# Optimization experiments

Measured on AMD Instinct MI355X. Metric: run time of the kernel, lower is better.

The kernel has to match this reference:

```python
import jax, jax.numpy as jnp
import numpy as np

N = 10000          # nodes
E = 200000         # edges (avg degree 20)
LAT = 128          # latent dim
NEXP = 8           # experts
NTYPE = 95         # atom types (hard-coded 95x0e in module)
M0, M1, M2 = 128, 64, 32          # node/out irreps muls for l=0,1,2 (dim 480)
E0, E1, E2 = 64, 32, 16           # edge irreps muls (dim 240)
C0, C1, C2 = M0 + E0, M1 + E1, M2 + E2   # concat channels per l
T0 = M0 + M1 + M2                 # gate-input scalars: 128 scalars + 96 gates
AVG_NEIGH = 20.0


def setup_inputs() -> dict:
    key = jax.random.key(0)
    ks = jax.random.split(key, 32)
    r = lambda i, sh: jax.random.normal(ks[i], sh, dtype=jnp.float32)
    return {
        "latents": r(0, (E, LAT)),
        "node_features": r(1, (N, M0 + 3 * M1 + 5 * M2)),
        "edge_features": r(2, (E, E0 + 3 * E1 + 5 * E2)),
        "edge_vector": r(3, (E, 3)),
        "mole_globals": r(4, (LAT,)),
        "wigner_D1": r(5, (E, 3, 3)),
        "wigner_D2": r(6, (E, 5, 5)),
        "node_onehot": jax.nn.one_hot(jax.random.randint(ks[7], (N,), 0, NTYPE), NTYPE, dtype=jnp.float32),
        "Wg": r(8, (LAT, NEXP)),
        "Wm": r(9, (LAT, NEXP)),
        "W0_e": r(10, (NEXP, C0, T0)), "W0_s": r(11, (C0, T0)),
        "W1_e": r(12, (NEXP, C1, M1)), "W1_s": r(13, (C1, M1)),
        "W2_e": r(14, (NEXP, C2, M2)), "W2_s": r(15, (C2, M2)),
        "Wp0": r(16, (M0, M0)), "bp0": jnp.zeros((M0,), jnp.float32),
        "Wp1": r(17, (M1, M1)), "Wp2": r(18, (M2, M2)),
        "Wenv": r(19, (LAT, M0 + M1 + M2)),
        "Woh0": r(20, (M0, NTYPE)), "Woh1": r(21, (M1, NTYPE)), "Woh2": r(22, (M2, NTYPE)),
        "atom_type": jax.random.randint(ks[23], (N,), 0, NTYPE),
        "edge_index": jax.random.randint(ks[24], (2, E), 0, N),
        "active_edges": jnp.arange(E),
    }


def _mix(x, We, Ws, g):
    """Latent(expert)-conditioned per-l channel mixing: y = x @ (sum_e g_e W_e + W_shared).
    Loops over the small fixed expert count; never materializes per-edge weight matrices."""
    xm = x if x.ndim == 3 else x[:, :, None]           # [a, c, m]
    y = jnp.einsum('acm,co->aom', xm, Ws)
    for e in range(NEXP):
        y = y + g[:, e, None, None] * jnp.einsum('acm,co->aom', xm, We[e])
    y = y * float(1.0 / np.sqrt(xm.shape[1]))
    return y[:, :, 0] if x.ndim == 2 else y


def reference(latents, node_features, edge_features, edge_vector, mole_globals,
              wigner_D1, wigner_D2, node_onehot, Wg, Wm,
              W0_e, W0_s, W1_e, W1_s, W2_e, W2_s,
              Wp0, bp0, Wp1, Wp2, Wenv, Woh0, Woh1, Woh2,
              atom_type, edge_index, active_edges):
    edge_center = edge_index[0][active_edges]
    lat = latents[active_edges]
    # gather node features along edges, split irreps blocks
    xn = node_features[edge_center]                         # [Ea, 480]
    n0 = xn[:, :M0]
    n1 = xn[:, M0:M0 + 3 * M1].reshape(-1, M1, 3)
    n2 = xn[:, M0 + 3 * M1:].reshape(-1, M2, 5)
    e0 = edge_features[:, :E0]
    e1 = edge_features[:, E0:E0 + 3 * E1].reshape(-1, E1, 3)
    e2 = edge_features[:, E0 + 3 * E1:].reshape(-1, E2, 5)
    x0 = jnp.concatenate([n0, e0], axis=1)                  # [Ea, C0]
    x1 = jnp.concatenate([n1, e1], axis=1)                  # [Ea, C1, 3]
    x2 = jnp.concatenate([n2, e2], axis=1)                  # [Ea, C2, 5]
    # latent + molecular-global conditioned expert gates
    gates = jax.nn.softmax(lat @ Wg + mole_globals @ Wm, axis=-1)   # [Ea, NEXP]
    # SO(2)-style TP: rotate l>0 blocks into edge frame (Wigner-D), mix channels, rotate back
    x1r = jnp.einsum('amn,acn->acm', wigner_D1, x1)
    x2r = jnp.einsum('amn,acn->acm', wigner_D2, x2)
    t0 = _mix(x0, W0_e, W0_s, gates)                        # [Ea, T0]
    t1 = jnp.einsum('anm,aom->aon', wigner_D1, _mix(x1r, W1_e, W1_s, gates))
    t2 = jnp.einsum('anm,aom->aon', wigner_D2, _mix(x2r, W2_e, W2_s, gates))
    # Gate nonlinearity: silu scalars, sigmoid gates scale l>0 channels
    s = jax.nn.silu(t0[:, :M0])
    v1 = t1 * jax.nn.sigmoid(t0[:, M0:M0 + M1])[:, :, None]
    v2 = t2 * jax.nn.sigmoid(t0[:, M0 + M1:])[:, :, None]
    # lin_post: per-l equivariant linear (bias only on scalars), fan-in normalized
    s = s @ Wp0 * float(1.0 / np.sqrt(M0)) + bp0
    v1 = jnp.einsum('acm,co->aom', v1, Wp1) * float(1.0 / np.sqrt(M1))
    v2 = jnp.einsum('acm,co->aom', v2, Wp2) * float(1.0 / np.sqrt(M2))
    # E3ElementLinear: per-channel weights generated from latents
    w = lat @ Wenv * float(1.0 / np.sqrt(LAT))              # [Ea, M0+M1+M2]
    s = s * w[:, :M0]
    v1 = v1 * w[:, M0:M0 + M1, None]
    v2 = v2 * w[:, M0 + M1:, None]
    # scatter-reduce messages to nodes, normalize by rsqrt(avg_num_neighbors)
    norm = float(1.0 / np.sqrt(AVG_NEIGH))
    o0 = jax.ops.segment_sum(s, edge_center, num_segments=N) * norm
    o1 = jax.ops.segment_sum(v1, edge_center, num_segments=N) * norm
    o2 = jax.ops.segment_sum(v2, edge_center, num_segments=N) * norm
    # residual blend (res_update_params=0 -> u=sigmoid(0)=0.5), identity residual
    u = 0.5
    c_old = float(1.0 / np.sqrt(u * u + 1.0))
    c_new = u * c_old
    h0 = c_old * node_features[:, :M0] + c_new * o0
    h1 = c_old * node_features[:, M0:M0 + 3 * M1].reshape(N, M1, 3) + c_new * o1
    h2 = c_old * node_features[:, M0 + 3 * M1:].reshape(N, M2, 5) + c_new * o2
    # layer-onehot 'uvu' weighted TP with 95x0e, fan-in normalized, added residually
    invs = float(1.0 / np.sqrt(NTYPE))
    h0 = h0 + h0 * (node_onehot @ Woh0.T) * invs
    h1 = h1 + h1 * (node_onehot @ Woh1.T)[:, :, None] * invs
    h2 = h2 + h2 * (node_onehot @ Woh2.T)[:, :, None] * invs
    return jnp.concatenate([h0, h1.reshape(N, 3 * M1), h2.reshape(N, 5 * M2)], axis=1)
```

## Files before the change

kernel.cpp:

```cpp
#include <hip/hip_runtime.h>
#include <math.h>

namespace {

typedef __attribute__((ext_vector_type(8))) short short8;
typedef __attribute__((ext_vector_type(4))) float f32x4;

constexpr int kN   = 10000;
constexpr int kE   = 200000;
constexpr int kNT  = 95;
constexpr int kNFD = 480;

__device__ __forceinline__ ushort bf(float f) {
  union { float f; uint u; } c; c.f = f;
  uint r = c.u + 0x7FFF + ((c.u >> 16) & 1);
  return (ushort)(r >> 16);
}
__device__ __forceinline__ float fb(ushort u) {
  union { uint u; float f; } c; c.u = ((uint)u) << 16;
  return c.f;
}
__device__ __forceinline__ uint pk2(float a, float b) {
  return (uint)bf(a) | ((uint)bf(b) << 16);
}

__device__ __forceinline__ void packone(int u, const float* We, const float* Ws,
                                        int expStride, int Kreal, int N, int NT,
                                        int NKp, ushort* d) {
  int i = u & 7;
  int lane = (u >> 3) & 63;
  int rest = u >> 9;
  int kc = rest % NKp; rest /= NKp;
  int nt = rest % NT;
  int e  = rest / NT;
  int k = kc*32 + (lane >> 4)*8 + i;
  int n = nt*16 + (lane & 15);
  float v = 0.f;
  if (k < Kreal) {
    const float* s = (Ws != nullptr && e == 8) ? Ws : (We + (size_t)e*expStride);
    v = s[(size_t)k*N + n];
  }
  d[u] = bf(v);
}

constexpr int PK0   = 0;
constexpr int PK1   = 387072;
constexpr int PK2   = 442368;
constexpr int PKENV = 460800;
constexpr int PKP0  = 489472;
constexpr int PKP1  = 505856;
constexpr int PKP2  = 509952;
constexpr int PKTOT = 510976;

__global__ __launch_bounds__(256)
void pack_k(const float* __restrict__ W0e, const float* __restrict__ W0s,
            const float* __restrict__ W1e, const float* __restrict__ W1s,
            const float* __restrict__ W2e, const float* __restrict__ W2s,
            const float* __restrict__ Wenv, const float* __restrict__ Wp0,
            const float* __restrict__ Wp1, const float* __restrict__ Wp2,
            ushort* __restrict__ dst) {
  int gid = blockIdx.x*256 + threadIdx.x;
  if (gid >= PKTOT) return;
  if (gid < PK1)        packone(gid - PK0,   W0e, W0s, 192*224, 192, 224, 14, 6, dst + PK0);
  else if (gid < PK2)   packone(gid - PK1,   W1e, W1s, 96*64,    96,  64,  4, 3, dst + PK1);
  else if (gid < PKENV) packone(gid - PK2,   W2e, W2s, 48*32,    48,  32,  2, 2, dst + PK2);
  else if (gid < PKP0)  packone(gid - PKENV, Wenv, nullptr, 0,  128, 224, 14, 4, dst + PKENV);
  else if (gid < PKP1)  packone(gid - PKP0,  Wp0, nullptr, 0,   128, 128,  8, 4, dst + PKP0);
  else if (gid < PKP2)  packone(gid - PKP1,  Wp1, nullptr, 0,    64,  64,  4, 2, dst + PKP1);
  else                  packone(gid - PKP2,  Wp2, nullptr, 0,    32,  32,  2, 1, dst + PKP2);
}

__global__ __launch_bounds__(64)
void mgl_k(const float* __restrict__ mgv, const float* __restrict__ Wm,
           float* __restrict__ mgl) {
  int x = threadIdx.x;
  if (x < 8) {
    float s = 0.f;
    for (int l = 0; l < 128; ++l) s += mgv[l]*Wm[l*8 + x];
    mgl[x] = s;
  }
}

__global__ __launch_bounds__(256)
void hist_k(const int* __restrict__ eidx, const int* __restrict__ act,
            int* __restrict__ counts) {
  int e = blockIdx.x*256 + threadIdx.x;
  if (e < kE) atomicAdd(&counts[eidx[act[e]]], 1);
}

__global__ __launch_bounds__(256)
void scan_k(const int* __restrict__ counts, int* __restrict__ rowptr,
            int* __restrict__ cursor) {
  __shared__ int part[256];
  const int t = threadIdx.x;
  const int start = t*40;
  int local = 0;
  for (int i = 0; i < 40; ++i) {
    int idx = start + i;
    if (idx < kN) local += counts[idx];
  }
  part[t] = local;
  __syncthreads();
  for (int ofs = 1; ofs < 256; ofs <<= 1) {
    int v = (t >= ofs) ? part[t - ofs] : 0;
    __syncthreads();
    part[t] += v;
    __syncthreads();
  }
  int run = part[t] - local;
  for (int i = 0; i < 40; ++i) {
    int idx = start + i;
    if (idx < kN) {
      rowptr[idx] = run;
      cursor[idx] = run;
      run += counts[idx];
    }
  }
  if (t == 255) rowptr[kN] = run;
}

__global__ __launch_bounds__(256)
void scatter_k(const int* __restrict__ eidx, const int* __restrict__ act,
               int* __restrict__ cursor, int* __restrict__ elist) {
  int e = blockIdx.x*256 + threadIdx.x;
  if (e < kE) {
    int n = eidx[act[e]];
    int pos = atomicAdd(&cursor[n], 1);
    elist[pos] = e;
  }
}

__global__ __launch_bounds__(256)
void prep_k(const float* __restrict__ latents, const float* __restrict__ nodef,
            const float* __restrict__ edgef, const float* __restrict__ mgl,
            const float* __restrict__ D1, const float* __restrict__ D2,
            const float* __restrict__ Wg,
            const int* __restrict__ eidx, const int* __restrict__ act,
            float* __restrict__ coefg,
            ushort* __restrict__ x0, ushort* __restrict__ x1r,
            ushort* __restrict__ x2r) {
  __shared__ int aidl[32], cenl[32];
  const int tid = threadIdx.x;
  const int base = blockIdx.x*32;

  if (tid < 32) {
    int a = act[base + tid];
    aidl[tid] = a;
    cenl[tid] = eidx[a];
  }
  __syncthreads();

  {
    int e = tid >> 3, x = tid & 7;
    const float* lat = latents + (size_t)aidl[e]*128;
    float s = mgl[x];
    for (int l = 0; l < 128; ++l) s += lat[l]*Wg[l*8 + x];
    float mx = s;
    mx = fmaxf(mx, __shfl_xor(mx, 1));
    mx = fmaxf(mx, __shfl_xor(mx, 2));
    mx = fmaxf(mx, __shfl_xor(mx, 4));
    float ex = __expf(s - mx);
    float sm = ex;
    sm += __shfl_xor(sm, 1);
    sm += __shfl_xor(sm, 2);
    sm += __shfl_xor(sm, 4);
    size_t a = base + e;
    coefg[a*9 + x] = ex/sm;
    if (x == 0) coefg[a*9 + 8] = 1.f;
  }

  for (int u = tid; u < 32*24; u += 256) {
    int e = u/24, g = u - e*24;
    int c0 = g*8;
    size_t a = base + e;
    const float* s = (g < 16) ? (nodef + (size_t)cenl[e]*kNFD + c0)
                              : (edgef + a*240 + (c0 - 128));
    float4 f0 = *(const float4*)s;
    float4 f1 = *(const float4*)(s + 4);
    uint4 o;
    o.x = pk2(f0.x, f0.y); o.y = pk2(f0.z, f0.w);
    o.z = pk2(f1.x, f1.y); o.w = pk2(f1.z, f1.w);
    *(uint4*)(x0 + a*192 + c0) = o;
  }

  for (int u = tid; u < 32*36; u += 256) {
    int e = u/36, r = u - e*36;
    int mm = r/12, g = r - mm*12;
    int c0 = g*8;
    size_t a = base + e;
    const float* dd = D1 + a*9 + mm*3;
    const float* s = (g < 8) ? (nodef + (size_t)cenl[e]*kNFD + 128 + c0*3)
                             : (edgef + a*240 + 64 + (c0 - 64)*3);
    float ld[24];
    #pragma unroll
    for (int q = 0; q < 6; ++q)
      *(float4*)(ld + q*4) = *(const float4*)(s + q*4);
    float d0 = dd[0], d1 = dd[1], d2 = dd[2];
    float ov[8];
    #pragma unroll
    for (int j = 0; j < 8; ++j)
      ov[j] = d0*ld[3*j] + d1*ld[3*j + 1] + d2*ld[3*j + 2];
    uint4 o;
    o.x = pk2(ov[0], ov[1]); o.y = pk2(ov[2], ov[3]);
    o.z = pk2(ov[4], ov[5]); o.w = pk2(ov[6], ov[7]);
    *(uint4*)(x1r + (a*3 + mm)*96 + c0) = o;
  }

  for (int u = tid; u < 32*40; u += 256) {
    int e = u/40, r = u - e*40;
    int mm = r >> 3, g = r & 7;
    int c0 = g*8;
    size_t a = base + e;
    uint4 o = {0u,0u,0u,0u};
    if (g < 6) {
      const float* dd = D2 + a*25 + mm*5;
      const float* s = (g < 4) ? (nodef + (size_t)cenl[e]*kNFD + 320 + c0*5)
                               : (edgef + a*240 + 160 + (c0 - 32)*5);
      float ld[40];
      #pragma unroll
      for (int q = 0; q < 10; ++q)
        *(float4*)(ld + q*4) = *(const float4*)(s + q*4);
      float d0 = dd[0], d1 = dd[1], d2 = dd[2], d3 = dd[3], d4 = dd[4];
      float ov[8];
      #pragma unroll
      for (int j = 0; j < 8; ++j)
        ov[j] = d0*ld[5*j] + d1*ld[5*j+1] + d2*ld[5*j+2] + d3*ld[5*j+3] + d4*ld[5*j+4];
      o.x = pk2(ov[0], ov[1]); o.y = pk2(ov[2], ov[3]);
      o.z = pk2(ov[4], ov[5]); o.w = pk2(ov[6], ov[7]);
    }
    *(uint4*)(x2r + (a*5 + mm)*64 + c0) = o;
  }
}

constexpr int gemm_smbytes(int K1, int NK, int N, int NEXP) {
  int LDA = K1 + 8;
  int NT = N/16;
  int a = 128*LDA*2;
  int b = NT*NK*1024;
  int u = a > b ? a : b;
  return u + (NEXP > 1 ? 128*NEXP*4 : 0);
}

template<int DIV, int K1, int NK, int N, int NEXP, int EPI, bool AF32>
__global__ __launch_bounds__(512)
void gemm_k(const ushort* __restrict__ A, const float* __restrict__ Af,
            const int* __restrict__ ridx, int strideA,
            const ushort* __restrict__ Bpk, const float* __restrict__ coefg,
            int rowsReal, float norm,
            ushort* __restrict__ outbf, const float* __restrict__ bias,
            const ushort* __restrict__ wenvbf, int WCOL) {
  constexpr int NT  = N/16;
  constexpr int CTW = NT/2;
  constexpr int LDA = K1 + 8;
  constexpr int ABYTES = 128*LDA*2;
  constexpr int BBYTES = NT*NK*1024;
  constexpr int UNI = (ABYTES > BBYTES) ? ABYTES : BBYTES;

  extern __shared__ char smraw[];
  ushort* Asm = (ushort*)smraw;
  float* coefsm = (float*)(smraw + UNI);

  const int tid = threadIdx.x;
  const int row0 = blockIdx.x*128;

  constexpr int C8 = K1/8;
  for (int u = tid; u < 128*C8; u += 512) {
    int r = u / C8, c8 = u - r*C8;
    int gr = row0 + r;
    uint4 v = {0u,0u,0u,0u};
    if (gr < rowsReal) {
      if constexpr (AF32) {
        const float* s = Af + (size_t)(ridx ? ridx[gr] : gr)*strideA + c8*8;
        float4 f0 = *(const float4*)s;
        float4 f1 = *(const float4*)(s + 4);
        v.x = pk2(f0.x, f0.y); v.y = pk2(f0.z, f0.w);
        v.z = pk2(f1.x, f1.y); v.w = pk2(f1.z, f1.w);
      } else {
        v = *(const uint4*)(A + (size_t)gr*strideA + c8*8);
      }
    }
    *(uint4*)(&Asm[r*LDA + c8*8]) = v;
  }
  if constexpr (NEXP > 1) {
    for (int u = tid; u < 128*NEXP; u += 512) {
      int r = u / NEXP, e = u - r*NEXP;
      int a = (row0 + r)/DIV;
      coefsm[r*NEXP + e] = coefg[(size_t)a*NEXP + e];
    }
  }
  __syncthreads();

  const int lane = tid & 63, wid = tid >> 6;
  const int cg = wid & 1, rg = wid >> 1;
  const int rbase = rg*32;
  const int lrow = lane & 15, lkb = lane >> 4;

  short8 af[2][NK];
  #pragma unroll
  for (int rt = 0; rt < 2; ++rt)
    #pragma unroll
    for (int kc = 0; kc < NK; ++kc)
      af[rt][kc] = *(const short8*)(&Asm[(rbase + rt*16 + lrow)*LDA + kc*32 + lkb*8]);

  f32x4 acc[2][CTW];
  #pragma unroll
  for (int rt = 0; rt < 2; ++rt)
    #pragma unroll
    for (int ct = 0; ct < CTW; ++ct)
      acc[rt][ct] = f32x4{0.f,0.f,0.f,0.f};

  __syncthreads();

  union BU { uint4 u; short8 s; };
  uint4* Bsm4 = (uint4*)smraw;
  const uint4* Bg4 = (const uint4*)Bpk;

  for (int e = 0; e < NEXP; ++e) {
    for (int u = tid; u < NT*NK*64; u += 512)
      Bsm4[u] = Bg4[(size_t)e*(NT*NK*64) + u];
    __syncthreads();

    if constexpr (NEXP > 1) {
      float cf[2][4];
      #pragma unroll
      for (int rt = 0; rt < 2; ++rt)
        #pragma unroll
        for (int q = 0; q < 4; ++q)
          cf[rt][q] = coefsm[(rbase + rt*16 + lkb*4 + q)*NEXP + e];
      #pragma unroll
      for (int ct = 0; ct < CTW; ++ct) {
        int nt = cg*CTW + ct;
        f32x4 z[2];
        z[0] = f32x4{0.f,0.f,0.f,0.f};
        z[1] = f32x4{0.f,0.f,0.f,0.f};
        #pragma unroll
        for (int kc = 0; kc < NK; ++kc) {
          BU b; b.u = Bsm4[(nt*NK + kc)*64 + lane];
          z[0] = __builtin_amdgcn_mfma_f32_16x16x32_bf16(af[0][kc], b.s, z[0], 0, 0, 0);
          z[1] = __builtin_amdgcn_mfma_f32_16x16x32_bf16(af[1][kc], b.s, z[1], 0, 0, 0);
        }
        #pragma unroll
        for (int q = 0; q < 4; ++q) {
          acc[0][ct][q] += cf[0][q]*z[0][q];
          acc[1][ct][q] += cf[1][q]*z[1][q];
        }
      }
    } else {
      #pragma unroll
      for (int ct = 0; ct < CTW; ++ct) {
        int nt = cg*CTW + ct;
        #pragma unroll
        for (int kc = 0; kc < NK; ++kc) {
          BU b; b.u = Bsm4[(nt*NK + kc)*64 + lane];
          acc[0][ct] = __builtin_amdgcn_mfma_f32_16x16x32_bf16(af[0][kc], b.s, acc[0][ct], 0, 0, 0);
          acc[1][ct] = __builtin_amdgcn_mfma_f32_16x16x32_bf16(af[1][kc], b.s, acc[1][ct], 0, 0, 0);
        }
      }
    }
    __syncthreads();
  }

  #pragma unroll
  for (int rt = 0; rt < 2; ++rt) {
    #pragma unroll
    for (int ct = 0; ct < CTW; ++ct) {
      #pragma unroll
      for (int q = 0; q < 4; ++q) {
        int gr = row0 + rbase + rt*16 + lkb*4 + q;
        if (gr >= rowsReal) continue;
        int o = (cg*CTW + ct)*16 + lrow;
        float val = acc[rt][ct][q]*norm;
        if constexpr (EPI == 0) {
          outbf[(size_t)gr*N + o] = bf(val);
        } else if constexpr (EPI == 1) {
          float av = (o < 128) ? (val/(1.f + __expf(-val)))
                               : (1.f/(1.f + __expf(-val)));
          outbf[(size_t)gr*N + o] = bf(av);
        } else {
          int a = gr/DIV;
          if (bias != nullptr) val += bias[o];
          float w = fb(wenvbf[(size_t)a*224 + WCOL + o]);
          val *= w*0.22360679774997896f;
          outbf[(size_t)gr*N + o] = bf(val);
        }
      }
    }
  }
}

__global__ __launch_bounds__(256)
void mid_k(const ushort* __restrict__ y1, const ushort* __restrict__ y2,
           const ushort* __restrict__ t0act, const float* __restrict__ D1,
           const float* __restrict__ D2, ushort* __restrict__ v1,
           ushort* __restrict__ v2) {
  const int base = blockIdx.x*64;
  const int tid = threadIdx.x;

  for (int u = tid; u < 64*24; u += 256) {
    int e = u/24, r = u - e*24;
    int n = r >> 3, g = r & 7;
    int c0 = g*8;
    size_t a = base + e;
    const float* dd = D1 + a*9 + n*3;
    float d0 = dd[0], d1 = dd[1], d2 = dd[2];
    short8 m0 = *(const short8*)(y1 + ((size_t)a*3 + 0)*64 + c0);
    short8 m1 = *(const short8*)(y1 + ((size_t)a*3 + 1)*64 + c0);
    short8 m2 = *(const short8*)(y1 + ((size_t)a*3 + 2)*64 + c0);
    short8 gt = *(const short8*)(t0act + a*224 + 128 + c0);
    float ov[8];
    #pragma unroll
    for (int j = 0; j < 8; ++j) {
      float s = d0*fb((ushort)m0[j]) + d1*fb((ushort)m1[j]) + d2*fb((ushort)m2[j]);
      ov[j] = s*fb((ushort)gt[j]);
    }
    uint4 o;
    o.x = pk2(ov[0], ov[1]); o.y = pk2(ov[2], ov[3]);
    o.z = pk2(ov[4], ov[5]); o.w = pk2(ov[6], ov[7]);
    *(uint4*)(v1 + ((size_t)a*3 + n)*64 + c0) = o;
  }

  for (int u = tid; u < 64*20; u += 256) {
    int e = u/20, r = u - e*20;
    int n = r >> 2, g = r & 3;
    int c0 = g*8;
    size_t a = base + e;
    const float* dd = D2 + a*25 + n*5;
    short8 m0 = *(const short8*)(y2 + ((size_t)a*5 + 0)*32 + c0);
    short8 m1 = *(const short8*)(y2 + ((size_t)a*5 + 1)*32 + c0);
    short8 m2 = *(const short8*)(y2 + ((size_t)a*5 + 2)*32 + c0);
    short8 m3 = *(const short8*)(y2 + ((size_t)a*5 + 3)*32 + c0);
    short8 m4 = *(const short8*)(y2 + ((size_t)a*5 + 4)*32 + c0);
    short8 gt = *(const short8*)(t0act + a*224 + 192 + c0);
    float ov[8];
    #pragma unroll
    for (int j = 0; j < 8; ++j) {
      float s = dd[0]*fb((ushort)m0[j]) + dd[1]*fb((ushort)m1[j])
              + dd[2]*fb((ushort)m2[j]) + dd[3]*fb((ushort)m3[j])
              + dd[4]*fb((ushort)m4[j]);
      ov[j] = s*fb((ushort)gt[j]);
    }
    uint4 o;
    o.x = pk2(ov[0], ov[1]); o.y = pk2(ov[2], ov[3]);
    o.z = pk2(ov[4], ov[5]); o.w = pk2(ov[6], ov[7]);
    *(uint4*)(v2 + ((size_t)a*5 + n)*32 + c0) = o;
  }
}

__global__ __launch_bounds__(256)
void gather_k(const float* __restrict__ nodef, const float* __restrict__ onehot,
              const float* __restrict__ Woh0, const float* __restrict__ Woh1,
              const float* __restrict__ Woh2,
              const int* __restrict__ rowptr, const int* __restrict__ elist,
              const ushort* __restrict__ pe0, const ushort* __restrict__ pe1,
              const ushort* __restrict__ pe2, float* __restrict__ out) {
  __shared__ int tn;
  const int n = blockIdx.x;
  const int t = threadIdx.x;
  if (t < kNT && onehot[(size_t)n*kNT + t] > 0.5f) tn = t;
  __syncthreads();
  const int ty = tn;
  const int r0 = rowptr[n], r1 = rowptr[n + 1];
  const float c_old = 0.8944271909999159f;
  const float c_new = 0.4472135954999579f;
  const float invs  = 0.10259783520851541f;

  for (int j = t; j < kNFD; j += 256) {
    int kind, row_m, col;
    if (j < 128)       { kind = 0; row_m = 0; col = j; }
    else if (j < 320)  { int jj = j - 128; col = jj/3; row_m = jj - col*3; kind = 1; }
    else               { int jj = j - 320; col = jj/5; row_m = jj - col*5; kind = 2; }

    float s = 0.f;
    for (int d = r0; d < r1; ++d) {
      int e = elist[d];
      ushort v;
      if (kind == 0)      v = pe0[(size_t)e*128 + col];
      else if (kind == 1) v = pe1[((size_t)e*3 + row_m)*64 + col];
      else                v = pe2[((size_t)e*5 + row_m)*32 + col];
      s += fb(v);
    }

    size_t idx = (size_t)n*kNFD + j;
    float h = c_old*nodef[idx] + c_new*s;
    float f;
    if (j < 128)      f = Woh0[j*kNT + ty];
    else if (j < 320) f = Woh1[((j - 128)/3)*kNT + ty];
    else              f = Woh2[((j - 320)/5)*kNT + ty];
    out[idx] = h*(1.f + f*invs);
  }
}

constexpr size_t OFF_CNT  = 0;
constexpr size_t OFF_CUR  = 40000;
constexpr size_t OFF_RP   = 80000;
constexpr size_t OFF_EL   = 120064;
constexpr size_t OFF_COEF = 19200000;
constexpr size_t OFF_MGL  = 26402304;
constexpr size_t OFF_X0   = 27202560;
constexpr size_t OFF_X1R  = 104027136;
constexpr size_t OFF_X2R  = 219264000;
constexpr size_t OFF_WENV = 347272192;
constexpr size_t OFF_T0A  = 436900864;
constexpr size_t OFF_Y1   = 526529536;
constexpr size_t OFF_Y2   = 603354112;
constexpr size_t OFF_PACK = 667358208;

}

extern "C" void kernel_launch(void* const* d_in, const int* in_sizes, int n_in,
                              void* d_out, int out_size, void* d_ws, size_t ws_size,
                              hipStream_t stream) {
  (void)in_sizes; (void)n_in; (void)out_size; (void)ws_size;
  const float* latents = (const float*)d_in[0];
  const float* nodef   = (const float*)d_in[1];
  const float* edgef   = (const float*)d_in[2];
  const float* mg      = (const float*)d_in[4];
  const float* D1      = (const float*)d_in[5];
  const float* D2      = (const float*)d_in[6];
  const float* onehot  = (const float*)d_in[7];
  const float* Wg      = (const float*)d_in[8];
  const float* Wm      = (const float*)d_in[9];
  const float* W0e     = (const float*)d_in[10];
  const float* W0s     = (const float*)d_in[11];
  const float* W1e     = (const float*)d_in[12];
  const float* W1s     = (const float*)d_in[13];
  const float* W2e     = (const float*)d_in[14];
  const float* W2s     = (const float*)d_in[15];
  const float* Wp0     = (const float*)d_in[16];
  const float* bp0     = (const float*)d_in[17];
  const float* Wp1     = (const float*)d_in[18];
  const float* Wp2     = (const float*)d_in[19];
  const float* Wenv    = (const float*)d_in[20];
  const float* Woh0    = (const float*)d_in[21];
  const float* Woh1    = (const float*)d_in[22];
  const float* Woh2    = (const float*)d_in[23];
  const int* eidx      = (const int*)d_in[25];
  const int* act       = (const int*)d_in[26];

  char* ws = (char*)d_ws;
  int*    cnt   = (int*)(ws + OFF_CNT);
  int*    cur   = (int*)(ws + OFF_CUR);
  int*    rp    = (int*)(ws + OFF_RP);
  int*    el    = (int*)(ws + OFF_EL);
  float*  coef  = (float*)(ws + OFF_COEF);
  float*  mgl   = (float*)(ws + OFF_MGL);
  ushort* x0    = (ushort*)(ws + OFF_X0);
  ushort* x1r   = (ushort*)(ws + OFF_X1R);
  ushort* x2r   = (ushort*)(ws + OFF_X2R);
  ushort* wenv  = (ushort*)(ws + OFF_WENV);
  ushort* t0act = (ushort*)(ws + OFF_T0A);
  ushort* y1    = (ushort*)(ws + OFF_Y1);
  ushort* y2    = (ushort*)(ws + OFF_Y2);
  ushort* v1    = (ushort*)(ws + OFF_X0);
  ushort* v2    = (ushort*)(ws + OFF_X1R);
  ushort* pe1   = (ushort*)(ws + OFF_X2R);
  ushort* pe2   = (ushort*)(ws + OFF_Y1);
  ushort* pe0   = (ushort*)(ws + OFF_Y2);
  ushort* pk    = (ushort*)(ws + OFF_PACK);
  float*  out   = (float*)d_out;

  hipMemsetAsync(cnt, 0, kN*sizeof(int), stream);
  hist_k<<<(kE + 255)/256, 256, 0, stream>>>(eidx, act, cnt);
  scan_k<<<1, 256, 0, stream>>>(cnt, rp, cur);
  scatter_k<<<(kE + 255)/256, 256, 0, stream>>>(eidx, act, cur, el);

  pack_k<<<(PKTOT + 255)/256, 256, 0, stream>>>(W0e, W0s, W1e, W1s, W2e, W2s,
                                                Wenv, Wp0, Wp1, Wp2, pk);
  mgl_k<<<1, 64, 0, stream>>>(mg, Wm, mgl);

  prep_k<<<kE/32, 256, 0, stream>>>(latents, nodef, edgef, mgl, D1, D2, Wg,
                                    eidx, act, coef, x0, x1r, x2r);

  {
    auto kp = gemm_k<1,192,6,224,9,1,false>;
    int smb = gemm_smbytes(192,6,224,9);
    hipFuncSetAttribute((const void*)kp, hipFuncAttributeMaxDynamicSharedMemorySize, smb);
    kp<<<1563, 512, smb, stream>>>(
        x0, nullptr, nullptr, 192, pk + PK0, coef, kE, 0.07216878364870323f,
        t0act, nullptr, nullptr, 0);
  }
  {
    auto kp = gemm_k<1,128,4,224,1,0,true>;
    int smb = gemm_smbytes(128,4,224,1);
    hipFuncSetAttribute((const void*)kp, hipFuncAttributeMaxDynamicSharedMemorySize, smb);
    kp<<<1563, 512, smb, stream>>>(
        nullptr, latents, act, 128, pk + PKENV, nullptr, kE, 0.08838834764831845f,
        wenv, nullptr, nullptr, 0);
  }
  {
    auto kp = gemm_k<3,96,3,64,9,0,false>;
    int smb = gemm_smbytes(96,3,64,9);
    hipFuncSetAttribute((const void*)kp, hipFuncAttributeMaxDynamicSharedMemorySize, smb);
    kp<<<4688, 512, smb, stream>>>(
        x1r, nullptr, nullptr, 96, pk + PK1, coef, 3*kE, 0.10206207261596577f,
        y1, nullptr, nullptr, 0);
  }
  {
    auto kp = gemm_k<5,64,2,32,9,0,false>;
    int smb = gemm_smbytes(64,2,32,9);
    hipFuncSetAttribute((const void*)kp, hipFuncAttributeMaxDynamicSharedMemorySize, smb);
    kp<<<7813, 512, smb, stream>>>(
        x2r, nullptr, nullptr, 64, pk + PK2, coef, 5*kE, 0.14433756729740643f,
        y2, nullptr, nullptr, 0);
  }

  mid_k<<<kE/64, 256, 0, stream>>>(y1, y2, t0act, D1, D2, v1, v2);

  {
    auto kp = gemm_k<1,128,4,128,1,2,false>;
    int smb = gemm_smbytes(128,4,128,1);
    hipFuncSetAttribute((const void*)kp, hipFuncAttributeMaxDynamicSharedMemorySize, smb);
    kp<<<1563, 512, smb, stream>>>(
        t0act, nullptr, nullptr, 224, pk + PKP0, nullptr, kE, 0.08838834764831845f,
        pe0, bp0, wenv, 0);
  }
  {
    auto kp = gemm_k<3,64,2,64,1,2,false>;
    int smb = gemm_smbytes(64,2,64,1);
    hipFuncSetAttribute((const void*)kp, hipFuncAttributeMaxDynamicSharedMemorySize, smb);
    kp<<<4688, 512, smb, stream>>>(
        v1, nullptr, nullptr, 64, pk + PKP1, nullptr, 3*kE, 0.125f,
        pe1, nullptr, wenv, 128);
  }
  {
    auto kp = gemm_k<5,32,1,32,1,2,false>;
    int smb = gemm_smbytes(32,1,32,1);
    hipFuncSetAttribute((const void*)kp, hipFuncAttributeMaxDynamicSharedMemorySize, smb);
    kp<<<7813, 512, smb, stream>>>(
        v2, nullptr, nullptr, 32, pk + PKP2, nullptr, 5*kE, 0.17677669529663687f,
        pe2, nullptr, wenv, 192);
  }

  gather_k<<<kN, 256, 0, stream>>>(nodef, onehot, Woh0, Woh1, Woh2,
                                   rp, el, pe0, pe1, pe2, out);
}
```

Before: 1.513 ms.

## Prefetch next expert weights into registers while computing current expert GEMM

```diff
diff --git a/kernel.cpp b/kernel.cpp
--- a/kernel.cpp
+++ b/kernel.cpp
@@ -242,7 +242,7 @@
 }
 
 template<int DIV, int K1, int NK, int N, int NEXP, int EPI, bool AF32>
-__global__ __launch_bounds__(512)
+__global__ __launch_bounds__(512, 2)
 void gemm_k(const ushort* __restrict__ A, const float* __restrict__ Af,
             const int* __restrict__ ridx, int strideA,
             const ushort* __restrict__ Bpk, const float* __restrict__ coefg,
@@ -255,6 +255,8 @@
   constexpr int ABYTES = 128*LDA*2;
   constexpr int BBYTES = NT*NK*1024;
   constexpr int UNI = (ABYTES > BBYTES) ? ABYTES : BBYTES;
+  constexpr int NB4 = NT*NK*64;
+  constexpr int NLD = (NB4 + 511)/512;
 
   extern __shared__ char smraw[];
   ushort* Asm = (ushort*)smraw;
@@ -262,6 +264,16 @@
 
   const int tid = threadIdx.x;
   const int row0 = blockIdx.x*128;
+
+  uint4* Bsm4 = (uint4*)smraw;
+  const uint4* Bg4 = (const uint4*)Bpk;
+  uint4 brg[NLD];
+
+  #pragma unroll
+  for (int i = 0; i < NLD; ++i) {
+    int u = tid + i*512;
+    if (u < NB4) brg[i] = Bg4[u];
+  }
 
   constexpr int C8 = K1/8;
   for (int u = tid; u < 128*C8; u += 512) {
@@ -311,14 +323,23 @@
 
   __syncthreads();
 
+  #pragma unroll
+  for (int i = 0; i < NLD; ++i) {
+    int u = tid + i*512;
+    if (u < NB4) Bsm4[u] = brg[i];
+  }
+  __syncthreads();
+
   union BU { uint4 u; short8 s; };
-  uint4* Bsm4 = (uint4*)smraw;
-  const uint4* Bg4 = (const uint4*)Bpk;
 
   for (int e = 0; e < NEXP; ++e) {
-    for (int u = tid; u < NT*NK*64; u += 512)
-      Bsm4[u] = Bg4[(size_t)e*(NT*NK*64) + u];
-    __syncthreads();
+    if (e + 1 < NEXP) {
+      #pragma unroll
+      for (int i = 0; i < NLD; ++i) {
+        int u = tid + i*512;
+        if (u < NB4) brg[i] = Bg4[(size_t)(e + 1)*NB4 + u];
+      }
+    }
 
     if constexpr (NEXP > 1) {
       float cf[2][4];
@@ -357,7 +378,16 @@
         }
       }
     }
-    __syncthreads();
+
+    if (e + 1 < NEXP) {
+      __syncthreads();
+      #pragma unroll
+      for (int i = 0; i < NLD; ++i) {
+        int u = tid + i*512;
+        if (u < NB4) Bsm4[u] = brg[i];
+      }
+      __syncthreads();
+    }
   }
 
   #pragma unroll
```

Result: slower. 1.795 ms (+18.7%).

## Add dedicated streaming-B MFMA kernel for the l=0 expert mixing GEMM

Applied to the files above, without the earlier changes.

```diff
diff --git a/kernel.cpp b/kernel.cpp
--- a/kernel.cpp
+++ b/kernel.cpp
@@ -25,8 +25,8 @@
 }
 
 __device__ __forceinline__ void packone(int u, const float* We, const float* Ws,
-                                        int expStride, int Kreal, int N, int NT,
-                                        int NKp, ushort* d) {
+                                        int expStride, int Kreal, int Nstride,
+                                        int Nreal, int NT, int NKp, ushort* d) {
   int i = u & 7;
   int lane = (u >> 3) & 63;
   int rest = u >> 9;
@@ -36,21 +36,21 @@
   int k = kc*32 + (lane >> 4)*8 + i;
   int n = nt*16 + (lane & 15);
   float v = 0.f;
-  if (k < Kreal) {
+  if (k < Kreal && n < Nreal) {
     const float* s = (Ws != nullptr && e == 8) ? Ws : (We + (size_t)e*expStride);
-    v = s[(size_t)k*N + n];
+    v = s[(size_t)k*Nstride + n];
   }
   d[u] = bf(v);
 }
 
 constexpr int PK0   = 0;
-constexpr int PK1   = 387072;
-constexpr int PK2   = 442368;
-constexpr int PKENV = 460800;
-constexpr int PKP0  = 489472;
-constexpr int PKP1  = 505856;
-constexpr int PKP2  = 509952;
-constexpr int PKTOT = 510976;
+constexpr int PK1   = 442368;
+constexpr int PK2   = 497664;
+constexpr int PKENV = 516096;
+constexpr int PKP0  = 544768;
+constexpr int PKP1  = 561152;
+constexpr int PKP2  = 565248;
+constexpr int PKTOT = 566272;
 
 __global__ __launch_bounds__(256)
 void pack_k(const float* __restrict__ W0e, const float* __restrict__ W0s,
@@ -61,13 +61,13 @@
             ushort* __restrict__ dst) {
   int gid = blockIdx.x*256 + threadIdx.x;
   if (gid >= PKTOT) return;
-  if (gid < PK1)        packone(gid - PK0,   W0e, W0s, 192*224, 192, 224, 14, 6, dst + PK0);
-  else if (gid < PK2)   packone(gid - PK1,   W1e, W1s, 96*64,    96,  64,  4, 3, dst + PK1);
-  else if (gid < PKENV) packone(gid - PK2,   W2e, W2s, 48*32,    48,  32,  2, 2, dst + PK2);
-  else if (gid < PKP0)  packone(gid - PKENV, Wenv, nullptr, 0,  128, 224, 14, 4, dst + PKENV);
-  else if (gid < PKP1)  packone(gid - PKP0,  Wp0, nullptr, 0,   128, 128,  8, 4, dst + PKP0);
-  else if (gid < PKP2)  packone(gid - PKP1,  Wp1, nullptr, 0,    64,  64,  4, 2, dst + PKP1);
-  else                  packone(gid - PKP2,  Wp2, nullptr, 0,    32,  32,  2, 1, dst + PKP2);
+  if (gid < PK1)        packone(gid - PK0,   W0e, W0s, 192*224, 192, 224, 224, 16, 6, dst + PK0);
+  else if (gid < PK2)   packone(gid - PK1,   W1e, W1s, 96*64,    96,  64,  64,  4, 3, dst + PK1);
+  else if (gid < PKENV) packone(gid - PK2,   W2e, W2s, 48*32,    48,  32,  32,  2, 2, dst + PK2);
+  else if (gid < PKP0)  packone(gid - PKENV, Wenv, nullptr, 0,  128, 224, 224, 14, 4, dst + PKENV);
+  else if (gid < PKP1)  packone(gid - PKP0,  Wp0, nullptr, 0,   128, 128, 128,  8, 4, dst + PKP0);
+  else if (gid < PKP2)  packone(gid - PKP1,  Wp1, nullptr, 0,    64,  64,  64,  4, 2, dst + PKP1);
+  else                  packone(gid - PKP2,  Wp2, nullptr, 0,    32,  32,  32,  2, 1, dst + PKP2);
 }
 
 __global__ __launch_bounds__(64)
@@ -388,6 +388,142 @@
   }
 }
 
+constexpr int T0SMB = 55808;
+
+template<int C>
+__device__ __forceinline__ void t0_phase(int e, int tid, int lane, int cg,
+                                         int rbase, int lkb,
+                                         const short8 (&af)[2][6],
+                                         f32x4 (&acc)[2][7],
+                                         const float* coefsm,
+                                         uint4* Bsm4, const uint4* Bg4,
+                                         uint4& rg0, uint4& rg1, uint4& rg2) {
+  __syncthreads();
+  const bool hasNext = !(e == 8 && C == 3);
+  if (hasNext) {
+    int ne = e + (C == 3 ? 1 : 0);
+    int nc = (C + 1) & 3;
+    const uint4* s = Bg4 + (size_t)ne*6144 + (size_t)nc*1536;
+    rg0 = s[tid]; rg1 = s[tid + 512]; rg2 = s[tid + 1024];
+  }
+  float cf[2][4];
+  #pragma unroll
+  for (int rt = 0; rt < 2; ++rt)
+    #pragma unroll
+    for (int q = 0; q < 4; ++q)
+      cf[rt][q] = coefsm[(rbase + rt*16 + lkb*4 + q)*9 + e];
+  union BU { uint4 u; short8 s; };
+  const uint4* bb = Bsm4 + (C & 1)*1536;
+  {
+    f32x4 z0 = {0.f,0.f,0.f,0.f}, z1 = {0.f,0.f,0.f,0.f};
+    #pragma unroll
+    for (int kc = 0; kc < 6; ++kc) {
+      BU b; b.u = bb[(cg*6 + kc)*64 + lane];
+      z0 = __builtin_amdgcn_mfma_f32_16x16x32_bf16(af[0][kc], b.s, z0, 0, 0, 0);
+      z1 = __builtin_amdgcn_mfma_f32_16x16x32_bf16(af[1][kc], b.s, z1, 0, 0, 0);
+    }
+    #pragma unroll
+    for (int q = 0; q < 4; ++q) {
+      acc[0][2*C][q] += cf[0][q]*z0[q];
+      acc[1][2*C][q] += cf[1][q]*z1[q];
+    }
+  }
+  if constexpr (2*C + 1 < 7) {
+    f32x4 z0 = {0.f,0.f,0.f,0.f}, z1 = {0.f,0.f,0.f,0.f};
+    #pragma unroll
+    for (int kc = 0; kc < 6; ++kc) {
+      BU b; b.u = bb[((2 + cg)*6 + kc)*64 + lane];
+      z0 = __builtin_amdgcn_mfma_f32_16x16x32_bf16(af[0][kc], b.s, z0, 0, 0, 0);
+      z1 = __builtin_amdgcn_mfma_f32_16x16x32_bf16(af[1][kc], b.s, z1, 0, 0, 0);
+    }
+    #pragma unroll
+    for (int q = 0; q < 4; ++q) {
+      acc[0][2*C + 1][q] += cf[0][q]*z0[q];
+      acc[1][2*C + 1][q] += cf[1][q]*z1[q];
+    }
+  }
+  __syncthreads();
+  if (hasNext) {
+    uint4* d = Bsm4 + ((C + 1) & 1)*1536;
+    d[tid] = rg0; d[tid + 512] = rg1; d[tid + 1024] = rg2;
+  }
+}
+
+__global__ __launch_bounds__(512, 2)
+void t0c_k(const ushort* __restrict__ A, const ushort* __restrict__ Bpk,
+           const float* __restrict__ coefg, ushort* __restrict__ outbf) {
+  extern __shared__ char smraw[];
+  ushort* Asm = (ushort*)smraw;
+  float* coefsm = (float*)(smraw + 51200);
+  uint4* Bsm4 = (uint4*)smraw;
+  const uint4* Bg4 = (const uint4*)Bpk;
+
+  const int tid = threadIdx.x;
+  const int row0 = blockIdx.x*128;
+
+  for (int u = tid; u < 128*24; u += 512) {
+    int r = u/24, c8 = u - r*24;
+    int gr = row0 + r;
+    uint4 v = {0u,0u,0u,0u};
+    if (gr < kE) v = *(const uint4*)(A + (size_t)gr*192 + c8*8);
+    *(uint4*)(&Asm[r*200 + c8*8]) = v;
+  }
+  for (int u = tid; u < 128*9; u += 512) {
+    int r = u/9, e = u - r*9;
+    coefsm[r*9 + e] = coefg[(size_t)(row0 + r)*9 + e];
+  }
+  __syncthreads();
+
+  const int lane = tid & 63, wid = tid >> 6;
+  const int cg = wid & 1, rg = wid >> 1;
+  const int rbase = rg*32;
+  const int lrow = lane & 15, lkb = lane >> 4;
+
+  short8 af[2][6];
+  #pragma unroll
+  for (int rt = 0; rt < 2; ++rt)
+    #pragma unroll
+    for (int kc = 0; kc < 6; ++kc)
+      af[rt][kc] = *(const short8*)(&Asm[(rbase + rt*16 + lrow)*200 + kc*32 + lkb*8]);
+
+  f32x4 acc[2][7];
+  #pragma unroll
+  for (int rt = 0; rt < 2; ++rt)
+    #pragma unroll
+    for (int ct = 0; ct < 7; ++ct)
+      acc[rt][ct] = f32x4{0.f,0.f,0.f,0.f};
+
+  __syncthreads();
+
+  uint4 rg0, rg1, rg2;
+  { const uint4* s = Bg4; rg0 = s[tid]; rg1 = s[tid + 512]; rg2 = s[tid + 1024]; }
+  { uint4* d = Bsm4;      d[tid] = rg0; d[tid + 512] = rg1; d[tid + 1024] = rg2; }
+
+  for (int e = 0; e < 9; ++e) {
+    t0_phase<0>(e, tid, lane, cg, rbase, lkb, af, acc, coefsm, Bsm4, Bg4, rg0, rg1, rg2);
+    t0_phase<1>(e, tid, lane, cg, rbase, lkb, af, acc, coefsm, Bsm4, Bg4, rg0, rg1, rg2);
+    t0_phase<2>(e, tid, lane, cg, rbase, lkb, af, acc, coefsm, Bsm4, Bg4, rg0, rg1, rg2);
+    t0_phase<3>(e, tid, lane, cg, rbase, lkb, af, acc, coefsm, Bsm4, Bg4, rg0, rg1, rg2);
+  }
+
+  #pragma unroll
+  for (int rt = 0; rt < 2; ++rt) {
+    #pragma unroll
+    for (int ct = 0; ct < 7; ++ct) {
+      #pragma unroll
+      for (int q = 0; q < 4; ++q) {
+        int gr = row0 + rbase + rt*16 + lkb*4 + q;
+        if (gr >= kE) continue;
+        int o = (2*ct + cg)*16 + lrow;
+        float val = acc[rt][ct][q]*0.07216878364870323f;
+        float av = (o < 128) ? (val/(1.f + __expf(-val)))
+                             : (1.f/(1.f + __expf(-val)));
+        outbf[(size_t)gr*224 + o] = bf(av);
+      }
+    }
+  }
+}
+
 __global__ __launch_bounds__(256)
 void mid_k(const ushort* __restrict__ y1, const ushort* __restrict__ y2,
            const ushort* __restrict__ t0act, const float* __restrict__ D1,
@@ -494,6 +630,7 @@
 constexpr size_t OFF_CUR  = 40000;
 constexpr size_t OFF_RP   = 80000;
 constexpr size_t OFF_EL   = 120064;
+constexpr size_t OFF_PACK = 1000000;
 constexpr size_t OFF_COEF = 19200000;
 constexpr size_t OFF_MGL  = 26402304;
 constexpr size_t OFF_X0   = 27202560;
@@ -503,7 +640,6 @@
 constexpr size_t OFF_T0A  = 436900864;
 constexpr size_t OFF_Y1   = 526529536;
 constexpr size_t OFF_Y2   = 603354112;
-constexpr size_t OFF_PACK = 667358208;
 
 }
 
@@ -542,6 +678,7 @@
   int*    cur   = (int*)(ws + OFF_CUR);
   int*    rp    = (int*)(ws + OFF_RP);
   int*    el    = (int*)(ws + OFF_EL);
+  ushort* pk    = (ushort*)(ws + OFF_PACK);
   float*  coef  = (float*)(ws + OFF_COEF);
   float*  mgl   = (float*)(ws + OFF_MGL);
   ushort* x0    = (ushort*)(ws + OFF_X0);
@@ -556,7 +693,6 @@
   ushort* pe1   = (ushort*)(ws + OFF_X2R);
   ushort* pe2   = (ushort*)(ws + OFF_Y1);
   ushort* pe0   = (ushort*)(ws + OFF_Y2);
-  ushort* pk    = (ushort*)(ws + OFF_PACK);
   float*  out   = (float*)d_out;
 
   hipMemsetAsync(cnt, 0, kN*sizeof(int), stream);
@@ -572,12 +708,9 @@
                                     eidx, act, coef, x0, x1r, x2r);
 
   {
-    auto kp = gemm_k<1,192,6,224,9,1,false>;
-    int smb = gemm_smbytes(192,6,224,9);
-    hipFuncSetAttribute((const void*)kp, hipFuncAttributeMaxDynamicSharedMemorySize, smb);
-    kp<<<1563, 512, smb, stream>>>(
-        x0, nullptr, nullptr, 192, pk + PK0, coef, kE, 0.07216878364870323f,
-        t0act, nullptr, nullptr, 0);
+    hipFuncSetAttribute((const void*)t0c_k,
+                        hipFuncAttributeMaxDynamicSharedMemorySize, T0SMB);
+    t0c_k<<<1563, 512, T0SMB, stream>>>(x0, pk + PK0, coef, t0act);
   }
   {
     auto kp = gemm_k<1,128,4,224,1,0,true>;
```

Measured after the change: 1.434 ms. 5.2% less time.
